# Kernel optimization log

Hardware: AMD Instinct MI355X
Metric: run time of the kernel (lower is better)

Reference implementation:

```python
import jax, jax.numpy as jnp
import numpy as np
import math

B, S, D, H = 4, 2048, 1024, 16
DH = D // H  # 64


def setup_inputs() -> dict:
    key = jax.random.key(0)
    ks = jax.random.split(key, 7)
    scale = 1.0 / math.sqrt(D)
    q = jax.random.normal(ks[0], (B, S, D), dtype=jnp.float32)
    k = jax.random.normal(ks[1], (B, S, D), dtype=jnp.float32)
    v = jax.random.normal(ks[2], (B, S, D), dtype=jnp.float32)
    mask = jnp.tril(jnp.ones((S, S), dtype=jnp.int32))[None, None]  # [1,1,S,S] causal
    wq = jax.random.normal(ks[3], (D, D), dtype=jnp.float32) * scale
    wk = jax.random.normal(ks[4], (D, D), dtype=jnp.float32) * scale
    wv = jax.random.normal(ks[5], (D, D), dtype=jnp.float32) * scale
    wo = jax.random.normal(ks[6], (D, D), dtype=jnp.float32) * scale
    return {"q": q, "k": k, "v": v, "mask": mask, "wq": wq, "wk": wk, "wv": wv, "wo": wo}


def reference(q, k, v, mask, wq, wk, wv, wo):
    # nn.Linear(bias=False): y = x @ W.T
    qry = q @ wq.T
    key = k @ wk.T
    val = v @ wv.T
    # [B,S,D] -> [B,H,S,DH]
    qry = qry.reshape(B, S, H, DH).transpose(0, 2, 1, 3)
    key = key.reshape(B, S, H, DH).transpose(0, 2, 1, 3)
    val = val.reshape(B, S, H, DH).transpose(0, 2, 1, 3)
    scores = jnp.einsum('bhqd,bhkd->bhqk', qry, key) / math.sqrt(DH)
    scores = jnp.where(mask == 0, jnp.float32(-1e9), scores)
    attn = jax.nn.softmax(scores, axis=-1)  # dropout p=0.0 -> identity
    x = jnp.einsum('bhqk,bhkd->bhqd', attn, val)
    x = x.transpose(0, 2, 1, 3).reshape(B, S, D)
    return x @ wo.T
```

## Files before the change

kernel.cpp:

```cpp
#include <hip/hip_runtime.h>
#include <hip/hip_bf16.h>

typedef __attribute__((ext_vector_type(8))) short bf16x8;
typedef __attribute__((ext_vector_type(4))) float f32x4;
typedef __attribute__((ext_vector_type(16))) float f32x16;

#define MFMA16(a, b, c) __builtin_amdgcn_mfma_f32_16x16x32_bf16((a), (b), (c), 0, 0, 0)
#define MFMA32(a, b, c) __builtin_amdgcn_mfma_f32_32x32x16_bf16((a), (b), (c), 0, 0, 0)

#if defined(__has_builtin)
#if __has_builtin(__builtin_amdgcn_exp2f)
#define EXP2(x) __builtin_amdgcn_exp2f(x)
#endif
#endif
#ifndef EXP2
#define EXP2(x) exp2f(x)
#endif

__device__ __forceinline__ short f2b(float f) {
  unsigned u = __builtin_bit_cast(unsigned, f);
  u += 0x7FFFu + ((u >> 16) & 1u);
  return (short)(u >> 16);
}
__device__ __forceinline__ unsigned cvtpk(float lo, float hi) {
  unsigned r;
  asm("v_cvt_pk_bf16_f32 %0, %1, %2" : "=v"(r) : "v"(lo), "v"(hi));
  return r;
}
__device__ __forceinline__ bf16x8 cvt8(float4 a, float4 b) {
  bf16x8 o;
  o[0] = f2b(a.x); o[1] = f2b(a.y); o[2] = f2b(a.z); o[3] = f2b(a.w);
  o[4] = f2b(b.x); o[5] = f2b(b.y); o[6] = f2b(b.z); o[7] = f2b(b.w);
  return o;
}

__global__ __launch_bounds__(256) void cvt4_bf16(const float* __restrict__ s0,
                                                 const float* __restrict__ s1,
                                                 const float* __restrict__ s2,
                                                 const float* __restrict__ s3,
                                                 short* __restrict__ d, long stride) {
  const int which = blockIdx.y;
  const float* s = which == 0 ? s0 : (which == 1 ? s1 : (which == 2 ? s2 : s3));
  long i = (long)blockIdx.x * 256 + threadIdx.x;
  const float4* sp = (const float4*)s;
  *(bf16x8*)(d + which * stride + i * 8) = cvt8(sp[2 * i], sp[2 * i + 1]);
}

template <int MODE>
__global__ __launch_bounds__(256) void gemm_proj(const float* __restrict__ A_,
                                                 const short* __restrict__ BT_,
                                                 short* __restrict__ Cout,
                                                 float oscale) {
  __shared__ __align__(16) short As[2][128 * 64];
  __shared__ __align__(16) short Bs[2][128 * 64];
  const int t = threadIdx.x;
  const int l = t & 63, w = t >> 6;
  const int grp = l >> 4, li = l & 15;
  const int wg = (((int)blockIdx.x & 7) << 6) | ((int)blockIdx.x >> 3);
  const int bm = wg >> 3, bn = wg & 7;
  const int m0 = bm << 7, n0 = bn << 7;
  const int wm = (w >> 1) << 6, wn = (w & 1) << 6;
  const int srow = t >> 3, scol = (t & 7) << 3;
  f32x4 acc[4][4] = {};

  {
#pragma unroll
    for (int i = 0; i < 4; ++i) {
      const float* ga = A_ + (long)(m0 + i * 32 + srow) * 1024 + scol;
      float4 a0 = *(const float4*)ga, a1 = *(const float4*)(ga + 4);
      *(bf16x8*)&As[0][i * 2048 + t * 8] = cvt8(a0, a1);
      const short* gb = BT_ + (long)(n0 + i * 32 + srow) * 1024 + scol;
      __builtin_amdgcn_global_load_lds(
          (const __attribute__((address_space(1))) void*)gb,
          (__attribute__((address_space(3))) void*)&Bs[0][i * 2048 + t * 8], 16, 0, 0);
    }
  }
  __syncthreads();
#pragma unroll 1
  for (int kt = 0; kt < 16; ++kt) {
    const int cur = kt & 1;
    float4 pf[4][2];
    if (kt + 1 < 16) {
#pragma unroll
      for (int i = 0; i < 4; ++i) {
        const float* ga = A_ + (long)(m0 + i * 32 + srow) * 1024 + (kt + 1) * 64 + scol;
        pf[i][0] = *(const float4*)ga;
        pf[i][1] = *(const float4*)(ga + 4);
        const short* gb = BT_ + (long)(n0 + i * 32 + srow) * 1024 + (kt + 1) * 64 + scol;
        __builtin_amdgcn_global_load_lds(
            (const __attribute__((address_space(1))) void*)gb,
            (__attribute__((address_space(3))) void*)&Bs[cur ^ 1][i * 2048 + t * 8], 16, 0, 0);
      }
    }
#pragma unroll
    for (int kk = 0; kk < 64; kk += 32) {
      bf16x8 af[4], bfr[4];
#pragma unroll
      for (int mi = 0; mi < 4; ++mi)
        af[mi] = *(const bf16x8*)&As[cur][(wm + mi * 16 + li) * 64 + kk + grp * 8];
#pragma unroll
      for (int ni = 0; ni < 4; ++ni)
        bfr[ni] = *(const bf16x8*)&Bs[cur][(wn + ni * 16 + li) * 64 + kk + grp * 8];
#pragma unroll
      for (int mi = 0; mi < 4; ++mi)
#pragma unroll
        for (int ni = 0; ni < 4; ++ni)
          acc[mi][ni] = MFMA16(af[mi], bfr[ni], acc[mi][ni]);
    }
    if (kt + 1 < 16) {
#pragma unroll
      for (int i = 0; i < 4; ++i)
        *(bf16x8*)&As[cur ^ 1][i * 2048 + t * 8] = cvt8(pf[i][0], pf[i][1]);
    }
    __syncthreads();
  }
#pragma unroll
  for (int mi = 0; mi < 4; ++mi) {
#pragma unroll
    for (int ni = 0; ni < 4; ++ni) {
      f32x4 v = acc[mi][ni];
      int n = n0 + wn + ni * 16 + li;
#pragma unroll
      for (int r = 0; r < 4; ++r) {
        int m = m0 + wm + mi * 16 + grp * 4 + r;
        int b = m >> 11, sq = m & 2047;
        int h = n >> 6, dh = n & 63;
        if (MODE == 0)
          Cout[(((long)(b * 16 + h) * 2048 + sq) << 6) + dh] = f2b(v[r] * oscale);
        else
          Cout[(((long)(b * 16 + h) * 64 + dh) << 11) + sq] = f2b(v[r]);
      }
    }
  }
}

__global__ __launch_bounds__(256) void gemm_out(const short* __restrict__ A_,
                                                const short* __restrict__ BT_,
                                                float* __restrict__ Cout) {
  __shared__ __align__(16) short As[2][128 * 64];
  __shared__ __align__(16) short Bs[2][128 * 64];
  const int t = threadIdx.x;
  const int l = t & 63, w = t >> 6;
  const int grp = l >> 4, li = l & 15;
  const int wg = (((int)blockIdx.x & 7) << 6) | ((int)blockIdx.x >> 3);
  const int bm = wg >> 3, bn = wg & 7;
  const int m0 = bm << 7, n0 = bn << 7;
  const int wm = (w >> 1) << 6, wn = (w & 1) << 6;
  const int srow = t >> 3, scol = (t & 7) << 3;
  f32x4 acc[4][4] = {};
#pragma unroll
  for (int i = 0; i < 4; ++i) {
    const short* ga = A_ + (long)(m0 + i * 32 + srow) * 1024 + scol;
    __builtin_amdgcn_global_load_lds(
        (const __attribute__((address_space(1))) void*)ga,
        (__attribute__((address_space(3))) void*)&As[0][i * 2048 + t * 8], 16, 0, 0);
    const short* gb = BT_ + (long)(n0 + i * 32 + srow) * 1024 + scol;
    __builtin_amdgcn_global_load_lds(
        (const __attribute__((address_space(1))) void*)gb,
        (__attribute__((address_space(3))) void*)&Bs[0][i * 2048 + t * 8], 16, 0, 0);
  }
  __syncthreads();
#pragma unroll 1
  for (int kt = 0; kt < 16; ++kt) {
    const int cur = kt & 1;
    if (kt + 1 < 16) {
#pragma unroll
      for (int i = 0; i < 4; ++i) {
        const short* ga = A_ + (long)(m0 + i * 32 + srow) * 1024 + (kt + 1) * 64 + scol;
        __builtin_amdgcn_global_load_lds(
            (const __attribute__((address_space(1))) void*)ga,
            (__attribute__((address_space(3))) void*)&As[cur ^ 1][i * 2048 + t * 8], 16, 0, 0);
        const short* gb = BT_ + (long)(n0 + i * 32 + srow) * 1024 + (kt + 1) * 64 + scol;
        __builtin_amdgcn_global_load_lds(
            (const __attribute__((address_space(1))) void*)gb,
            (__attribute__((address_space(3))) void*)&Bs[cur ^ 1][i * 2048 + t * 8], 16, 0, 0);
      }
    }
#pragma unroll
    for (int kk = 0; kk < 64; kk += 32) {
      bf16x8 af[4], bfr[4];
#pragma unroll
      for (int mi = 0; mi < 4; ++mi)
        af[mi] = *(const bf16x8*)&As[cur][(wm + mi * 16 + li) * 64 + kk + grp * 8];
#pragma unroll
      for (int ni = 0; ni < 4; ++ni)
        bfr[ni] = *(const bf16x8*)&Bs[cur][(wn + ni * 16 + li) * 64 + kk + grp * 8];
#pragma unroll
      for (int mi = 0; mi < 4; ++mi)
#pragma unroll
        for (int ni = 0; ni < 4; ++ni)
          acc[mi][ni] = MFMA16(af[mi], bfr[ni], acc[mi][ni]);
    }
    __syncthreads();
  }
#pragma unroll
  for (int mi = 0; mi < 4; ++mi) {
#pragma unroll
    for (int ni = 0; ni < 4; ++ni) {
      f32x4 v = acc[mi][ni];
      int n = n0 + wn + ni * 16 + li;
#pragma unroll
      for (int r = 0; r < 4; ++r) {
        int m = m0 + wm + mi * 16 + grp * 4 + r;
        Cout[(long)m * 1024 + n] = v[r];
      }
    }
  }
}

__device__ __forceinline__ void attn_tile(const short* Kbuf, const short* Vbuf,
                                          const bf16x8 qf[4], f32x16& oa, f32x16& ob,
                                          float& mrun, float& lsum, int kt, bool diag,
                                          int khmax, int qg, int q, int hi) {
  f32x16 p0 = {}, p1 = {};
  __builtin_amdgcn_s_setprio(1);
#pragma unroll
  for (int kd = 0; kd < 4; ++kd) {
    int colB = kd * 32 + hi * 16;
    bf16x8 kf0 = *(const bf16x8*)((const char*)Kbuf + q * 128 + (colB ^ ((q & 7) << 4)));
    p0 = MFMA32(kf0, qf[kd], p0);
  }
  if (khmax == 2) {
#pragma unroll
    for (int kd = 0; kd < 4; ++kd) {
      int colB = kd * 32 + hi * 16;
      bf16x8 kf1 = *(const bf16x8*)((const char*)Kbuf + (q + 32) * 128 + (colB ^ ((q & 7) << 4)));
      p1 = MFMA32(kf1, qf[kd], p1);
    }
  }
  __builtin_amdgcn_s_setprio(0);
  if (diag) {
#pragma unroll
    for (int r = 0; r < 16; ++r) {
      int key0 = kt * 64 + (r & 3) + 8 * (r >> 2) + 4 * hi;
      if (key0 > qg) p0[r] = -1e30f;
      if (key0 + 32 > qg) p1[r] = -1e30f;
    }
  }
  float pm = p0[0];
#pragma unroll
  for (int r = 1; r < 16; ++r) pm = fmaxf(pm, p0[r]);
  if (khmax == 2) {
#pragma unroll
    for (int r = 0; r < 16; ++r) pm = fmaxf(pm, p1[r]);
  }
  pm = fmaxf(pm, __shfl_xor(pm, 32));
  const bool skip = __all(pm - mrun <= 11.5f);
  float mn;
  float alpha = 1.f;
  if (skip) {
    mn = mrun;
  } else {
    mn = fmaxf(mrun, pm);
    alpha = EXP2(mrun - mn);
    mrun = mn;
  }
  float ts = 0.f;
#pragma unroll
  for (int r = 0; r < 16; ++r) { p0[r] = EXP2(p0[r] - mn); ts += p0[r]; }
  if (khmax == 2) {
#pragma unroll
    for (int r = 0; r < 16; ++r) { p1[r] = EXP2(p1[r] - mn); ts += p1[r]; }
  }
  ts += __shfl_xor(ts, 32);
  if (skip) {
    lsum += ts;
  } else {
    lsum = lsum * alpha + ts;
#pragma unroll
    for (int r = 0; r < 16; ++r) { oa[r] *= alpha; ob[r] *= alpha; }
  }
  unsigned own0[8], prt0[8], own1[8], prt1[8];
#pragma unroll
  for (int g = 0; g < 4; ++g) {
    own0[2 * g]     = cvtpk(p0[4 * g], p0[4 * g + 1]);
    own0[2 * g + 1] = cvtpk(p0[4 * g + 2], p0[4 * g + 3]);
  }
#pragma unroll
  for (int i = 0; i < 8; ++i) prt0[i] = __shfl_xor(own0[i], 32);
  if (khmax == 2) {
#pragma unroll
    for (int g = 0; g < 4; ++g) {
      own1[2 * g]     = cvtpk(p1[4 * g], p1[4 * g + 1]);
      own1[2 * g + 1] = cvtpk(p1[4 * g + 2], p1[4 * g + 3]);
    }
#pragma unroll
    for (int i = 0; i < 8; ++i) prt1[i] = __shfl_xor(own1[i], 32);
  }
  __builtin_amdgcn_s_setprio(1);
#define PVSTEP(KD, OWN, PRT)                                                              \
  {                                                                                       \
    const int kdl = (KD) & 1;                                                             \
    unsigned b0 = hi ? PRT[4 * kdl + 2] : OWN[4 * kdl];                                   \
    unsigned b1 = hi ? PRT[4 * kdl + 3] : OWN[4 * kdl + 1];                               \
    unsigned b2 = hi ? OWN[4 * kdl + 2] : PRT[4 * kdl];                                   \
    unsigned b3 = hi ? OWN[4 * kdl + 3] : PRT[4 * kdl + 1];                               \
    int4 bi = {(int)b0, (int)b1, (int)b2, (int)b3};                                       \
    bf16x8 pb = __builtin_bit_cast(bf16x8, bi);                                           \
    int colB = (KD) * 32 + hi * 16;                                                       \
    bf16x8 vf0 = *(const bf16x8*)((const char*)Vbuf + q * 128 + (colB ^ ((q & 7) << 4))); \
    bf16x8 vf1 = *(const bf16x8*)((const char*)Vbuf + (q + 32) * 128 + (colB ^ ((q & 7) << 4))); \
    oa = MFMA32(vf0, pb, oa);                                                             \
    ob = MFMA32(vf1, pb, ob);                                                             \
  }
  PVSTEP(0, own0, prt0);
  PVSTEP(1, own0, prt0);
  if (khmax == 2) {
    PVSTEP(2, own1, prt1);
    PVSTEP(3, own1, prt1);
  }
#undef PVSTEP
  __builtin_amdgcn_s_setprio(0);
}

__global__ __launch_bounds__(256, 2) void attn_fwd(const short* __restrict__ Qh,
                                                   const short* __restrict__ Kh,
                                                   const short* __restrict__ Vt,
                                                   short* __restrict__ Xb) {
  __shared__ __align__(16) short Ks[2][4096];
  __shared__ __align__(16) short Vs[2][4096];
  const int bh = blockIdx.x;
  const int qtA = blockIdx.y;
  const int qtB = 15 - qtA;
  const int t = threadIdx.x, l = t & 63, w = t >> 6;
  const int q = l & 31, hi = l >> 5;
  const int q0wA = qtA * 128 + w * 32, q0wB = qtB * 128 + w * 32;
  const int qgA = q0wA + q, qgB = q0wB + q;
  const short* Qp = Qh + (long)bh * 131072;
  const char* Kb = (const char*)(Kh + (long)bh * 131072);
  const char* Vb = (const char*)(Vt + (long)bh * 131072);

  bf16x8 qfA[4], qfB[4];
#pragma unroll
  for (int kd = 0; kd < 4; ++kd) {
    qfA[kd] = *(const bf16x8*)(Qp + (long)qgA * 64 + kd * 16 + hi * 8);
    qfB[kd] = *(const bf16x8*)(Qp + (long)qgB * 64 + kd * 16 + hi * 8);
  }

  const int co0 = t * 16, co1 = co0 + 4096;

  f32x16 oaA = {}, obA = {}, oaB = {}, obB = {};
  float mrunA = -1e30f, lsumA = 0.f, mrunB = -1e30f, lsumB = 0.f;
  const int tripsA = (q0wA >> 6) + 1;
  const int tripsB = (q0wB >> 6) + 1;
  const int nt = 2 * qtB + 2;

#define STAGE(KT, BUF)                                                                   \
  {                                                                                      \
    long ktb = (long)(KT) * 8192;                                                        \
    _Pragma("unroll") for (int c = 0; c < 2; ++c) {                                      \
      int o = c ? co1 : co0;                                                             \
      int ksrc = o ^ (((o >> 7) & 7) << 4);                                              \
      __builtin_amdgcn_global_load_lds(                                                  \
          (const __attribute__((address_space(1))) void*)(Kb + ktb + ksrc),              \
          (__attribute__((address_space(3))) void*)((char*)Ks[BUF] + o), 16, 0, 0);      \
      int row = o >> 7, c16 = (o >> 4) & 7;                                              \
      int vsrc = row * 4096 + (KT) * 128 + (((c16 ^ (row & 7))) << 4);                   \
      __builtin_amdgcn_global_load_lds(                                                  \
          (const __attribute__((address_space(1))) void*)(Vb + vsrc),                    \
          (__attribute__((address_space(3))) void*)((char*)Vs[BUF] + o), 16, 0, 0);      \
    }                                                                                    \
  }

  STAGE(0, 0);
  __syncthreads();

  for (int kt = 0; kt < nt; ++kt) {
    const int buf = kt & 1;
    if (kt + 1 < nt) STAGE(kt + 1, buf ^ 1);

    if (kt < tripsB) {
      const bool diag = (kt == tripsB - 1);
      const int khmax = (diag && ((q0wB & 32) == 0)) ? 1 : 2;
      attn_tile(Ks[buf], Vs[buf], qfB, oaB, obB, mrunB, lsumB, kt, diag, khmax, qgB, q, hi);
    }
    if (kt < tripsA) {
      const bool diag = (kt == tripsA - 1);
      const int khmax = (diag && ((q0wA & 32) == 0)) ? 1 : 2;
      attn_tile(Ks[buf], Vs[buf], qfA, oaA, obA, mrunA, lsumA, kt, diag, khmax, qgA, q, hi);
    }
    __syncthreads();
  }

  const int b = bh >> 4, h = bh & 15;
#define EPI(OA, OB, LS, QG)                                                \
  {                                                                        \
    const float inv = 1.f / (LS);                                          \
    short* orow = Xb + (long)(b * 2048 + (QG)) * 1024 + h * 64;            \
    _Pragma("unroll") for (int g = 0; g < 4; ++g) {                        \
      unsigned u0 = cvtpk((OA)[4 * g] * inv, (OA)[4 * g + 1] * inv);       \
      unsigned u1 = cvtpk((OA)[4 * g + 2] * inv, (OA)[4 * g + 3] * inv);   \
      uint2 uu = {u0, u1};                                                 \
      *(uint2*)(orow + 8 * g + 4 * hi) = uu;                               \
      unsigned w0 = cvtpk((OB)[4 * g] * inv, (OB)[4 * g + 1] * inv);       \
      unsigned w1 = cvtpk((OB)[4 * g + 2] * inv, (OB)[4 * g + 3] * inv);   \
      uint2 ww = {w0, w1};                                                 \
      *(uint2*)(orow + 32 + 8 * g + 4 * hi) = ww;                          \
    }                                                                      \
  }
  EPI(oaA, obA, lsumA, qgA);
  EPI(oaB, obB, lsumB, qgB);
#undef EPI
}

extern "C" void kernel_launch(void* const* d_in, const int* in_sizes, int n_in,
                              void* d_out, int out_size, void* d_ws, size_t ws_size,
                              hipStream_t stream) {
  const float* q  = (const float*)d_in[0];
  const float* k  = (const float*)d_in[1];
  const float* v  = (const float*)d_in[2];
  const float* wq = (const float*)d_in[4];
  const float* wk = (const float*)d_in[5];
  const float* wv = (const float*)d_in[6];
  const float* wo = (const float*)d_in[7];

  short* ws = (short*)d_ws;
  const long T = 8388608;
  short* Qh  = ws;
  short* Kh  = Qh + T;
  short* Vt  = Kh + T;
  short* Xb  = Vt + T;
  short* wqb = Xb + T;
  short* wkb = wqb + 1048576;
  short* wvb = wkb + 1048576;
  short* wob = wvb + 1048576;

  cvt4_bf16<<<dim3(512, 4), 256, 0, stream>>>(wq, wk, wv, wo, wqb, 1048576);

  gemm_proj<0><<<512, 256, 0, stream>>>(q, wqb, Qh, 0.18033688f);
  gemm_proj<0><<<512, 256, 0, stream>>>(k, wkb, Kh, 1.0f);
  gemm_proj<1><<<512, 256, 0, stream>>>(v, wvb, Vt, 1.0f);
  attn_fwd<<<dim3(64, 8), 256, 0, stream>>>(Qh, Kh, Vt, Xb);
  gemm_out<<<512, 256, 0, stream>>>(Xb, wob, (float*)d_out);
}
```

Baseline: 201.1 us.

## Single-buffer LDS in projection and output GEMMs to raise occupancy

Replaces the double-buffered LDS tiles (64 KB per block) with single buffers (32 KB) in both GEMM kernels. In gemm_proj the B tile is now prefetched into registers alongside A and written to LDS after a barrier, instead of going directly to LDS asynchronously. In gemm_out the prefetch is dropped entirely: each k-step loads straight to LDS, waits on a barrier, then computes. The aim is more resident blocks per CU to hide latency, at the cost of extra barriers, lost load/compute overlap in gemm_out, and more register use for the B prefetch in gemm_proj.

```diff
diff --git a/kernel.cpp b/kernel.cpp
--- a/kernel.cpp
+++ b/kernel.cpp
@@ -51,8 +51,8 @@
                                                  const short* __restrict__ BT_,
                                                  short* __restrict__ Cout,
                                                  float oscale) {
-  __shared__ __align__(16) short As[2][128 * 64];
-  __shared__ __align__(16) short Bs[2][128 * 64];
+  __shared__ __align__(16) short As[128 * 64];
+  __shared__ __align__(16) short Bs[128 * 64];
   const int t = threadIdx.x;
   const int l = t & 63, w = t >> 6;
   const int grp = l >> 4, li = l & 15;
@@ -63,57 +63,54 @@
   const int srow = t >> 3, scol = (t & 7) << 3;
   f32x4 acc[4][4] = {};
 
-  {
-#pragma unroll
-    for (int i = 0; i < 4; ++i) {
-      const float* ga = A_ + (long)(m0 + i * 32 + srow) * 1024 + scol;
-      float4 a0 = *(const float4*)ga, a1 = *(const float4*)(ga + 4);
-      *(bf16x8*)&As[0][i * 2048 + t * 8] = cvt8(a0, a1);
-      const short* gb = BT_ + (long)(n0 + i * 32 + srow) * 1024 + scol;
-      __builtin_amdgcn_global_load_lds(
-          (const __attribute__((address_space(1))) void*)gb,
-          (__attribute__((address_space(3))) void*)&Bs[0][i * 2048 + t * 8], 16, 0, 0);
-    }
-  }
+  float4 pa[4][2];
+  bf16x8 pb[4];
+#define PLOAD(KT)                                                            \
+  {                                                                          \
+    _Pragma("unroll") for (int i = 0; i < 4; ++i) {                          \
+      const float* ga = A_ + (long)(m0 + i * 32 + srow) * 1024 + (KT) * 64 + scol; \
+      pa[i][0] = *(const float4*)ga;                                         \
+      pa[i][1] = *(const float4*)(ga + 4);                                   \
+      pb[i] = *(const bf16x8*)(BT_ + (long)(n0 + i * 32 + srow) * 1024 + (KT) * 64 + scol); \
+    }                                                                        \
+  }
+#define PWRITE()                                                             \
+  {                                                                          \
+    _Pragma("unroll") for (int i = 0; i < 4; ++i) {                          \
+      *(bf16x8*)&As[i * 2048 + t * 8] = cvt8(pa[i][0], pa[i][1]);            \
+      *(bf16x8*)&Bs[i * 2048 + t * 8] = pb[i];                               \
+    }                                                                        \
+  }
+
+  PLOAD(0);
+  PWRITE();
   __syncthreads();
 #pragma unroll 1
   for (int kt = 0; kt < 16; ++kt) {
-    const int cur = kt & 1;
-    float4 pf[4][2];
-    if (kt + 1 < 16) {
-#pragma unroll
-      for (int i = 0; i < 4; ++i) {
-        const float* ga = A_ + (long)(m0 + i * 32 + srow) * 1024 + (kt + 1) * 64 + scol;
-        pf[i][0] = *(const float4*)ga;
-        pf[i][1] = *(const float4*)(ga + 4);
-        const short* gb = BT_ + (long)(n0 + i * 32 + srow) * 1024 + (kt + 1) * 64 + scol;
-        __builtin_amdgcn_global_load_lds(
-            (const __attribute__((address_space(1))) void*)gb,
-            (__attribute__((address_space(3))) void*)&Bs[cur ^ 1][i * 2048 + t * 8], 16, 0, 0);
-      }
-    }
+    if (kt + 1 < 16) PLOAD(kt + 1);
 #pragma unroll
     for (int kk = 0; kk < 64; kk += 32) {
       bf16x8 af[4], bfr[4];
 #pragma unroll
       for (int mi = 0; mi < 4; ++mi)
-        af[mi] = *(const bf16x8*)&As[cur][(wm + mi * 16 + li) * 64 + kk + grp * 8];
+        af[mi] = *(const bf16x8*)&As[(wm + mi * 16 + li) * 64 + kk + grp * 8];
 #pragma unroll
       for (int ni = 0; ni < 4; ++ni)
-        bfr[ni] = *(const bf16x8*)&Bs[cur][(wn + ni * 16 + li) * 64 + kk + grp * 8];
+        bfr[ni] = *(const bf16x8*)&Bs[(wn + ni * 16 + li) * 64 + kk + grp * 8];
 #pragma unroll
       for (int mi = 0; mi < 4; ++mi)
 #pragma unroll
         for (int ni = 0; ni < 4; ++ni)
           acc[mi][ni] = MFMA16(af[mi], bfr[ni], acc[mi][ni]);
     }
+    __syncthreads();
     if (kt + 1 < 16) {
-#pragma unroll
-      for (int i = 0; i < 4; ++i)
-        *(bf16x8*)&As[cur ^ 1][i * 2048 + t * 8] = cvt8(pf[i][0], pf[i][1]);
-    }
-    __syncthreads();
-  }
+      PWRITE();
+      __syncthreads();
+    }
+  }
+#undef PLOAD
+#undef PWRITE
 #pragma unroll
   for (int mi = 0; mi < 4; ++mi) {
 #pragma unroll
@@ -137,8 +134,8 @@
 __global__ __launch_bounds__(256) void gemm_out(const short* __restrict__ A_,
                                                 const short* __restrict__ BT_,
                                                 float* __restrict__ Cout) {
-  __shared__ __align__(16) short As[2][128 * 64];
-  __shared__ __align__(16) short Bs[2][128 * 64];
+  __shared__ __align__(16) short As[128 * 64];
+  __shared__ __align__(16) short Bs[128 * 64];
   const int t = threadIdx.x;
   const int l = t & 63, w = t >> 6;
   const int grp = l >> 4, li = l & 15;
@@ -148,43 +145,29 @@
   const int wm = (w >> 1) << 6, wn = (w & 1) << 6;
   const int srow = t >> 3, scol = (t & 7) << 3;
   f32x4 acc[4][4] = {};
-#pragma unroll
-  for (int i = 0; i < 4; ++i) {
-    const short* ga = A_ + (long)(m0 + i * 32 + srow) * 1024 + scol;
-    __builtin_amdgcn_global_load_lds(
-        (const __attribute__((address_space(1))) void*)ga,
-        (__attribute__((address_space(3))) void*)&As[0][i * 2048 + t * 8], 16, 0, 0);
-    const short* gb = BT_ + (long)(n0 + i * 32 + srow) * 1024 + scol;
-    __builtin_amdgcn_global_load_lds(
-        (const __attribute__((address_space(1))) void*)gb,
-        (__attribute__((address_space(3))) void*)&Bs[0][i * 2048 + t * 8], 16, 0, 0);
-  }
-  __syncthreads();
 #pragma unroll 1
   for (int kt = 0; kt < 16; ++kt) {
-    const int cur = kt & 1;
-    if (kt + 1 < 16) {
-#pragma unroll
-      for (int i = 0; i < 4; ++i) {
-        const short* ga = A_ + (long)(m0 + i * 32 + srow) * 1024 + (kt + 1) * 64 + scol;
-        __builtin_amdgcn_global_load_lds(
-            (const __attribute__((address_space(1))) void*)ga,
-            (__attribute__((address_space(3))) void*)&As[cur ^ 1][i * 2048 + t * 8], 16, 0, 0);
-        const short* gb = BT_ + (long)(n0 + i * 32 + srow) * 1024 + (kt + 1) * 64 + scol;
-        __builtin_amdgcn_global_load_lds(
-            (const __attribute__((address_space(1))) void*)gb,
-            (__attribute__((address_space(3))) void*)&Bs[cur ^ 1][i * 2048 + t * 8], 16, 0, 0);
-      }
-    }
+#pragma unroll
+    for (int i = 0; i < 4; ++i) {
+      const short* ga = A_ + (long)(m0 + i * 32 + srow) * 1024 + kt * 64 + scol;
+      __builtin_amdgcn_global_load_lds(
+          (const __attribute__((address_space(1))) void*)ga,
+          (__attribute__((address_space(3))) void*)&As[i * 2048 + t * 8], 16, 0, 0);
+      const short* gb = BT_ + (long)(n0 + i * 32 + srow) * 1024 + kt * 64 + scol;
+      __builtin_amdgcn_global_load_lds(
+          (const __attribute__((address_space(1))) void*)gb,
+          (__attribute__((address_space(3))) void*)&Bs[i * 2048 + t * 8], 16, 0, 0);
+    }
+    __syncthreads();
 #pragma unroll
     for (int kk = 0; kk < 64; kk += 32) {
       bf16x8 af[4], bfr[4];
 #pragma unroll
       for (int mi = 0; mi < 4; ++mi)
-        af[mi] = *(const bf16x8*)&As[cur][(wm + mi * 16 + li) * 64 + kk + grp * 8];
+        af[mi] = *(const bf16x8*)&As[(wm + mi * 16 + li) * 64 + kk + grp * 8];
 #pragma unroll
       for (int ni = 0; ni < 4; ++ni)
-        bfr[ni] = *(const bf16x8*)&Bs[cur][(wn + ni * 16 + li) * 64 + kk + grp * 8];
+        bfr[ni] = *(const bf16x8*)&Bs[(wn + ni * 16 + li) * 64 + kk + grp * 8];
 #pragma unroll
       for (int mi = 0; mi < 4; ++mi)
 #pragma unroll
```

Measured after the change: 199.2 us (median of 3 runs). About the same (-1.0%).
